# Optimization experiments

Measured on AMD Instinct MI355X. Metric: run time of the kernel, lower is better.

Reference implementation:

```python
import jax, jax.numpy as jnp
import numpy as np

INPUT = 28
HID = 64
OUT = 10


def setup_inputs() -> dict:
    key = jax.random.key(0)
    ks = jax.random.split(key, 8)
    s_ih = 1.0 / np.sqrt(HID)
    x = jax.random.normal(ks[0], (16384, 28, INPUT), dtype=jnp.float32)
    # PyTorch LSTM params: gate order (i, f, g, o), each block of size HID
    W_ih = jax.random.uniform(ks[1], (4 * HID, INPUT), jnp.float32, -s_ih, s_ih)
    W_hh = jax.random.uniform(ks[2], (4 * HID, HID), jnp.float32, -s_ih, s_ih)
    b_ih = jax.random.uniform(ks[3], (4 * HID,), jnp.float32, -s_ih, s_ih)
    b_hh = jax.random.uniform(ks[4], (4 * HID,), jnp.float32, -s_ih, s_ih)
    s_fc = 1.0 / np.sqrt(HID)
    W_fc = jax.random.uniform(ks[5], (OUT, HID), jnp.float32, -s_fc, s_fc)
    b_fc = jax.random.uniform(ks[6], (OUT,), jnp.float32, -s_fc, s_fc)
    return {"x": x, "W_ih": W_ih, "W_hh": W_hh, "b_ih": b_ih, "b_hh": b_hh,
            "W_fc": W_fc, "b_fc": b_fc}


def reference(x, W_ih, W_hh, b_ih, b_hh, W_fc, b_fc):
    B = x.shape[0]
    # Precompute input projections for all timesteps in one big GEMM: [T, B, 4H]
    x_proj = jnp.einsum('bti,gi->tbg', x, W_ih) + (b_ih + b_hh)

    def step(carry, xp_t):
        h, c = carry
        gates = xp_t + h @ W_hh.T  # [B, 4H]
        i, f, g, o = jnp.split(gates, 4, axis=-1)
        i = jax.nn.sigmoid(i)
        f = jax.nn.sigmoid(f)
        g = jnp.tanh(g)
        o = jax.nn.sigmoid(o)
        c = f * c + i * g
        h = o * jnp.tanh(c)
        return (h, c), None

    h0 = jnp.zeros((B, HID), dtype=x.dtype)
    c0 = jnp.zeros((B, HID), dtype=x.dtype)
    (h_last, _), _ = jax.lax.scan(step, (h0, c0), x_proj)
    # fc on the last timestep's hidden state (== output[:, -1, :])
    return h_last @ W_fc.T + b_fc
```

## Files before the change

### kernel.cpp

```cpp
#include <hip/hip_runtime.h>
#include <hip/hip_bf16.h>


namespace {
constexpr int B_TOT   = 16384;
constexpr int T_STEPS = 28;
constexpr int IN_DIM  = 28;
constexpr int HID     = 64;
constexpr int OUT_DIM = 10;
constexpr int ROWS    = 16;
constexpr int THREADS = 256;
constexpr int KP      = 104;
constexpr int XROW    = T_STEPS * IN_DIM;
constexpr int NFRAG   = 16 * 3;
constexpr int WS_ELEMS = NFRAG * 64 * 8;
}

typedef __attribute__((ext_vector_type(8))) short short8v;
typedef __attribute__((ext_vector_type(4))) short short4v;
typedef __attribute__((ext_vector_type(4))) float float4v;

__device__ __forceinline__ short f2bf_cold(float f) {
  union { float f; unsigned u; } v; v.f = f;
  unsigned r = v.u + 0x7FFFu + ((v.u >> 16) & 1u);
  return (short)(r >> 16);
}
__device__ __forceinline__ float bf2f(short s) {
  union { unsigned u; float f; } v; v.u = ((unsigned)(unsigned short)s) << 16;
  return v.f;
}
__device__ __forceinline__ unsigned pk2(float a, float b) {
  __hip_bfloat162 h = __float22bfloat162_rn(float2{a, b});
  union { __hip_bfloat162 h; unsigned u; } cv; cv.h = h; return cv.u;
}

__global__ void lstm_prep(const float* __restrict__ W_ih,
                          const float* __restrict__ W_hh,
                          const float* __restrict__ b_ih,
                          const float* __restrict__ b_hh,
                          unsigned short* __restrict__ ws) {
  int idx = blockIdx.x * blockDim.x + threadIdx.x;
  if (idx >= WS_ELEMS) return;
  int j  = idx & 7;
  int l  = (idx >> 3) & 63;
  int fk = idx >> 9;
  int kc = fk % 3;
  int mt = fk / 3;
  int m  = 16 * mt + (l & 15);
  int unit = m >> 2, type = m & 3;
  int g  = type * 64 + unit;
  int k  = kc * 32 + (l >> 4) * 8 + j;
  float v = 0.0f;
  if (k < IN_DIM)        v = W_ih[g * IN_DIM + k];
  else if (k == IN_DIM)  v = b_ih[g] + b_hh[g];
  else if (k >= 32)      v = W_hh[g * HID + (k - 32)];
  ws[idx] = (unsigned short)f2bf_cold(v);
}

__global__ __attribute__((amdgpu_flat_work_group_size(THREADS, THREADS),
                          amdgpu_waves_per_eu(4, 4)))
void lstm_mfma8(const float* __restrict__ x,
                const unsigned short* __restrict__ wfrag,
                const float* __restrict__ W_fc,
                const float* __restrict__ b_fc, float* __restrict__ out) {
  __shared__ short hs[2][ROWS][KP];

  const int tid  = threadIdx.x;
  const int lane = tid & 63;
  const int w    = tid >> 6;
  const int l15  = lane & 15;
  const int q    = lane >> 4;
  const int b0   = blockIdx.x * ROWS;

  short8v a[4][3];
#pragma unroll
  for (int i = 0; i < 4; ++i)
#pragma unroll
    for (int kc = 0; kc < 3; ++kc)
      a[i][kc] = *(const short8v*)&wfrag[((((4 * w + i) * 3) + kc) * 64 + lane) * 8];

  for (int idx = tid; idx < 2 * ROWS * KP; idx += THREADS) (&hs[0][0][0])[idx] = 0;
  __syncthreads();
  if (tid < 2 * ROWS) hs[tid >> 4][tid & 15][IN_DIM] = (short)0x3F80;

  const bool stager = (lane < 28);
  const int  s  = w * 28 + lane;
  const int  sr = s / 7;
  const int  sc = s - 7 * sr;
  const float* xptr = x + (size_t)(b0 + sr) * XROW + sc * 4;

  float4 xfly = {0.f, 0.f, 0.f, 0.f};
  if (stager) {
    float4 x0 = *(const float4*)xptr;
    short4v sv;
    unsigned plo = pk2(x0.x, x0.y), phi = pk2(x0.z, x0.w);
    sv[0] = (short)(plo & 0xFFFF); sv[1] = (short)(plo >> 16);
    sv[2] = (short)(phi & 0xFFFF); sv[3] = (short)(phi >> 16);
    *(short4v*)&hs[0][sr][sc * 4] = sv;
    xfly = *(const float4*)(xptr + 1 * IN_DIM);
  }
  __syncthreads();

  float c_state[4] = {0.f, 0.f, 0.f, 0.f};

  for (int t = 0; t < T_STEPS; ++t) {
    const int cur = t & 1, nxt = cur ^ 1;

    short8v bf0 = *(const short8v*)&hs[cur][l15][q * 8];
    short8v bf1 = *(const short8v*)&hs[cur][l15][32 + q * 8];
    short8v bf2 = *(const short8v*)&hs[cur][l15][64 + q * 8];

    if (stager) {
      if (t + 1 < T_STEPS) {
        short4v sv;
        unsigned plo = pk2(xfly.x, xfly.y), phi = pk2(xfly.z, xfly.w);
        sv[0] = (short)(plo & 0xFFFF); sv[1] = (short)(plo >> 16);
        sv[2] = (short)(phi & 0xFFFF); sv[3] = (short)(phi >> 16);
        *(short4v*)&hs[nxt][sr][sc * 4] = sv;
      }
      if (t + 2 < T_STEPS)
        xfly = *(const float4*)(xptr + (t + 2) * IN_DIM);
    }

    const float4v zero4 = {0.f, 0.f, 0.f, 0.f};
    float4v acc[4];
#pragma unroll
    for (int i = 0; i < 4; ++i)
      acc[i] = __builtin_amdgcn_mfma_f32_16x16x32_bf16(a[i][0], bf0, zero4, 0, 0, 0);
#pragma unroll
    for (int i = 0; i < 4; ++i)
      acc[i] = __builtin_amdgcn_mfma_f32_16x16x32_bf16(a[i][1], bf1, acc[i], 0, 0, 0);
#pragma unroll
    for (int i = 0; i < 4; ++i)
      acc[i] = __builtin_amdgcn_mfma_f32_16x16x32_bf16(a[i][2], bf2, acc[i], 0, 0, 0);

    float hv[4];
#pragma unroll
    for (int i = 0; i < 4; ++i) {
      float4v g4 = acc[i];
      float Ei = __expf(-g4[0]);
      float Ef = __expf(-g4[1]);
      float Eg = __expf(-2.0f * g4[2]);
      float Eo = __expf(-g4[3]);
      float di = 1.0f + Ei, df = 1.0f + Ef;
      float r1 = __builtin_amdgcn_rcpf(di * df);
      float iv = r1 * df;
      float fv = r1 * di;
      float gv = fmaf(2.0f, __builtin_amdgcn_rcpf(1.0f + Eg), -1.0f);
      float cn = fmaf(fv, c_state[i], iv * gv);
      c_state[i] = cn;
      float ct = fminf(fmaxf(cn, -15.0f), 15.0f);
      float Ec = __expf(-2.0f * ct);
      float dn = 1.0f + Eo, dc = 1.0f + Ec;
      float r2 = __builtin_amdgcn_rcpf(dn * dc);
      float ov = r2 * dc;
      float tc = fmaf(2.0f * r2, dn, -1.0f);
      hv[i] = ov * tc;
    }
    unsigned p01 = pk2(hv[0], hv[1]);
    unsigned p23 = pk2(hv[2], hv[3]);
    hs[nxt][l15][32 + 16 * w + 0 + q]  = (short)(p01 & 0xFFFF);
    hs[nxt][l15][32 + 16 * w + 4 + q]  = (short)(p01 >> 16);
    hs[nxt][l15][32 + 16 * w + 8 + q]  = (short)(p23 & 0xFFFF);
    hs[nxt][l15][32 + 16 * w + 12 + q] = (short)(p23 >> 16);

    __syncthreads();
  }

  if (tid < ROWS * OUT_DIM) {
    const int r = tid / OUT_DIM;
    const int o = tid - r * OUT_DIM;
    float sacc = b_fc[o];
#pragma unroll
    for (int j = 0; j < HID; ++j)
      sacc += bf2f(hs[0][r][32 + j]) * W_fc[o * HID + j];
    out[(b0 + r) * OUT_DIM + o] = sacc;
  }
}

extern "C" void kernel_launch(void* const* d_in, const int* in_sizes, int n_in,
                              void* d_out, int out_size, void* d_ws, size_t ws_size,
                              hipStream_t stream) {
  const float* x    = (const float*)d_in[0];
  const float* W_ih = (const float*)d_in[1];
  const float* W_hh = (const float*)d_in[2];
  const float* b_ih = (const float*)d_in[3];
  const float* b_hh = (const float*)d_in[4];
  const float* W_fc = (const float*)d_in[5];
  const float* b_fc = (const float*)d_in[6];
  float* out = (float*)d_out;
  unsigned short* ws = (unsigned short*)d_ws;

  lstm_prep<<<(WS_ELEMS + 255) / 256, 256, 0, stream>>>(W_ih, W_hh, b_ih, b_hh, ws);

  dim3 grid(B_TOT / ROWS);
  dim3 block(THREADS);
  lstm_mfma8<<<grid, block, 0, stream>>>(x, ws, W_fc, b_fc, out);
}
```

Baseline: 132.3 us.

## Fold log2e scaling into weights, share reciprocals, vectorize hidden-state LDS store

The prep kernel pre-multiplies the gate weights by log2(e), or by 2*log2(e) for the g gate, so the cell can use raw exp2 with no per-element scaling. It also merges three reciprocals into one shared rcp per unit. The W_hh columns and the FC weights are permuted so each lane's four hidden values sit contiguously in LDS, which turns four scalar short stores into one 8-byte store. This cuts transcendental and VALU work and LDS store instructions on the serial recurrence path. In exchange it adds bf16 rounding of the scaled weights and a wider tanh clamp, which could slightly change accuracy.

Measured after the change: 134.2 us. About the same (+1.4%).

```diff
diff --git a/kernel.cpp b/kernel.cpp
--- a/kernel.cpp
+++ b/kernel.cpp
@@ -12,8 +12,7 @@
 constexpr int THREADS = 256;
 constexpr int KP      = 104;
 constexpr int XROW    = T_STEPS * IN_DIM;
-constexpr int NFRAG   = 16 * 3;
-constexpr int WS_ELEMS = NFRAG * 64 * 8;
+constexpr int WS_ELEMS = 48 * 64 * 8;
 }
 
 typedef __attribute__((ext_vector_type(8))) short short8v;
@@ -53,13 +52,18 @@
   float v = 0.0f;
   if (k < IN_DIM)        v = W_ih[g * IN_DIM + k];
   else if (k == IN_DIM)  v = b_ih[g] + b_hh[g];
-  else if (k >= 32)      v = W_hh[g * HID + (k - 32)];
+  else if (k >= 32) {
+    int p = k - 32;
+    int u = 16 * (p >> 4) + 4 * (p & 3) + ((p >> 2) & 3);
+    v = W_hh[g * HID + u];
+  }
+  v *= (type == 2) ? 2.8853900817779268f : 1.4426950408889634f;
   ws[idx] = (unsigned short)f2bf_cold(v);
 }
 
 __global__ __attribute__((amdgpu_flat_work_group_size(THREADS, THREADS),
                           amdgpu_waves_per_eu(4, 4)))
-void lstm_mfma8(const float* __restrict__ x,
+void lstm_mfma9(const float* __restrict__ x,
                 const unsigned short* __restrict__ wfrag,
                 const float* __restrict__ W_fc,
                 const float* __restrict__ b_fc, float* __restrict__ out) {
@@ -138,31 +142,32 @@
 #pragma unroll
     for (int i = 0; i < 4; ++i) {
       float4v g4 = acc[i];
-      float Ei = __expf(-g4[0]);
-      float Ef = __expf(-g4[1]);
-      float Eg = __expf(-2.0f * g4[2]);
-      float Eo = __expf(-g4[3]);
-      float di = 1.0f + Ei, df = 1.0f + Ef;
-      float r1 = __builtin_amdgcn_rcpf(di * df);
-      float iv = r1 * df;
-      float fv = r1 * di;
-      float gv = fmaf(2.0f, __builtin_amdgcn_rcpf(1.0f + Eg), -1.0f);
+      float Ei = __builtin_amdgcn_exp2f(-g4[0]);
+      float Ef = __builtin_amdgcn_exp2f(-g4[1]);
+      float Eg = __builtin_amdgcn_exp2f(-g4[2]);
+      float di = 1.0f + Ei, df = 1.0f + Ef, dg = 1.0f + Eg;
+      float t1 = di * df;
+      float r1 = __builtin_amdgcn_rcpf(t1 * dg);
+      float iv = r1 * (df * dg);
+      float fv = r1 * (di * dg);
+      float gnum = fmaf(-Eg, 2.8853900817779268f, 2.8853900817779268f);
+      float gv = (r1 * t1) * gnum;
       float cn = fmaf(fv, c_state[i], iv * gv);
       c_state[i] = cn;
-      float ct = fminf(fmaxf(cn, -15.0f), 15.0f);
-      float Ec = __expf(-2.0f * ct);
+      float ct = fminf(fmaxf(cn, -44.0f), 44.0f);
+      float Eo = __builtin_amdgcn_exp2f(-g4[3]);
+      float Ec = __builtin_amdgcn_exp2f(-ct);
       float dn = 1.0f + Eo, dc = 1.0f + Ec;
       float r2 = __builtin_amdgcn_rcpf(dn * dc);
       float ov = r2 * dc;
-      float tc = fmaf(2.0f * r2, dn, -1.0f);
+      float tc = (r2 * dn) * (1.0f - Ec);
       hv[i] = ov * tc;
     }
     unsigned p01 = pk2(hv[0], hv[1]);
     unsigned p23 = pk2(hv[2], hv[3]);
-    hs[nxt][l15][32 + 16 * w + 0 + q]  = (short)(p01 & 0xFFFF);
-    hs[nxt][l15][32 + 16 * w + 4 + q]  = (short)(p01 >> 16);
-    hs[nxt][l15][32 + 16 * w + 8 + q]  = (short)(p23 & 0xFFFF);
-    hs[nxt][l15][32 + 16 * w + 12 + q] = (short)(p23 >> 16);
+    union { unsigned u[2]; short4v s; } pw;
+    pw.u[0] = p01; pw.u[1] = p23;
+    *(short4v*)&hs[nxt][l15][32 + 16 * w + 4 * q] = pw.s;
 
     __syncthreads();
   }
@@ -172,8 +177,10 @@
     const int o = tid - r * OUT_DIM;
     float sacc = b_fc[o];
 #pragma unroll
-    for (int j = 0; j < HID; ++j)
-      sacc += bf2f(hs[0][r][32 + j]) * W_fc[o * HID + j];
+    for (int p = 0; p < HID; ++p) {
+      const int u = 16 * (p >> 4) + 4 * (p & 3) + ((p >> 2) & 3);
+      sacc += bf2f(hs[0][r][32 + p]) * W_fc[o * HID + u];
+    }
     out[(b0 + r) * OUT_DIM + o] = sacc;
   }
 }
@@ -195,5 +202,5 @@
 
   dim3 grid(B_TOT / ROWS);
   dim3 block(THREADS);
-  lstm_mfma8<<<grid, block, 0, stream>>>(x, ws, W_fc, b_fc, out);
-}
+  lstm_mfma9<<<grid, block, 0, stream>>>(x, ws, W_fc, b_fc, out);
+}
```
